# Optimization experiments

Measured on AMD Instinct MI355X. Metric: run time of the kernel, lower is better.

The kernel has to match this reference:

```python
import jax, jax.numpy as jnp
import numpy as np

N = 20000
E = 320000
IN_FEAT = 256
HID = 256
OUT_FEAT = 128


def setup_inputs() -> dict:
    key = jax.random.key(0)
    ks = jax.random.split(key, 10)
    inp = {
        "x": jax.random.normal(ks[0], (N, IN_FEAT), dtype=jnp.float32),
        "edge_src": jax.random.randint(ks[1], (E,), 0, N, dtype=jnp.int32),
        "edge_dst": jax.random.randint(ks[2], (E,), 0, N, dtype=jnp.int32),
        "edge_w": jax.random.uniform(ks[3], (E,), dtype=jnp.float32),
        # params (Linear weights stored as [out, in], torch convention)
        "W_emb": jax.random.normal(ks[4], (HID, IN_FEAT), dtype=jnp.float32) / np.sqrt(IN_FEAT),
        "W_gc1": jax.random.normal(ks[5], (HID, 2 * HID), dtype=jnp.float32) / np.sqrt(2 * HID),
        "b_gc1": jnp.zeros((HID,), dtype=jnp.float32),
        "W_gc2": jax.random.normal(ks[6], (HID, 2 * HID), dtype=jnp.float32) / np.sqrt(2 * HID),
        "b_gc2": jnp.zeros((HID,), dtype=jnp.float32),
        "W_fc": jax.random.normal(ks[7], (OUT_FEAT, HID), dtype=jnp.float32) / np.sqrt(HID),
    }
    return inp


def reference(x, edge_src, edge_dst, edge_w, W_emb, W_gc1, b_gc1, W_gc2, b_gc2, W_fc):
    n = x.shape[0]

    def adj_mul(h):
        msgs = h[edge_src] * edge_w[:, None]           # [E, hid]
        return jax.ops.segment_sum(msgs, edge_dst, num_segments=n)

    def gconv(h, W, b):
        cat = jnp.concatenate([h, adj_mul(h)], axis=1)  # [N, 2*hid]
        return cat @ W.T + b

    h = x @ W_emb.T                                    # embedding (no bias)
    h = h + jax.nn.relu(gconv(h, W_gc1, b_gc1))        # residual (dropout = eval identity)
    h = h + jax.nn.relu(gconv(h, W_gc2, b_gc2))
    out = h @ W_fc.T                                   # fc_last (no bias)
    out = out / jnp.sqrt(jnp.sum(out * out, axis=1, keepdims=True))
    return out
```

## Files before the change

### kernel.cpp

```cpp
#include <hip/hip_runtime.h>
#include <math.h>

#define N_NODES 20000
#define E_EDGES 320000
#define HID 256
#define OUT_FEAT 128
#define MPAD 20224
#define CAP 64

#define BK 64
#define LSTR 72
#define ISTR 80
#define TSTR 264

typedef __attribute__((ext_vector_type(8))) __bf16 bf16x8;
typedef __attribute__((ext_vector_type(4))) float floatx4;
typedef __attribute__((ext_vector_type(4))) int intx4;

__device__ __forceinline__ void write_int8_shadow64(
    const __bf16 (*tile)[TSTR], int row0, int tid,
    unsigned char* __restrict__ h8, float* __restrict__ scl) {
    const int row = tid >> 3;
    const int seg = tid & 7;
    float vals[32];
    float mx = 0.f;
#pragma unroll
    for (int j = 0; j < 32; j++) {
        float v = (float)tile[row][seg * 32 + j];
        vals[j] = v;
        mx = fmaxf(mx, fabsf(v));
    }
#pragma unroll
    for (int m = 1; m <= 4; m <<= 1) mx = fmaxf(mx, __shfl_xor(mx, m));
    const float enc = mx > 0.f ? 127.f / mx : 0.f;
    unsigned int pk[8];
#pragma unroll
    for (int g = 0; g < 8; g++) {
        unsigned int wd = 0;
#pragma unroll
        for (int j = 0; j < 4; j++) {
            int q = (int)rintf(vals[g * 4 + j] * enc);
            q = q > 127 ? 127 : (q < -127 ? -127 : q);
            wd |= ((unsigned int)(q & 0xff)) << (8 * j);
        }
        pk[g] = wd;
    }
    unsigned char* dstp = h8 + (size_t)(row0 + row) * HID + seg * 32;
    *(int4*)dstp        = make_int4(pk[0], pk[1], pk[2], pk[3]);
    *(int4*)(dstp + 16) = make_int4(pk[4], pk[5], pk[6], pk[7]);
    if (seg == 0) scl[row0 + row] = mx * (1.f / 127.f);
}

__device__ __forceinline__ void write_int8_shadow32(
    const __bf16 (*tile)[TSTR], int row0, int tid,
    unsigned char* __restrict__ h8, float* __restrict__ scl) {
    const int row = tid >> 4;
    const int seg = tid & 15;
    float vals[16];
    float mx = 0.f;
#pragma unroll
    for (int j = 0; j < 16; j++) {
        float v = (float)tile[row][seg * 16 + j];
        vals[j] = v;
        mx = fmaxf(mx, fabsf(v));
    }
#pragma unroll
    for (int m = 1; m <= 8; m <<= 1) mx = fmaxf(mx, __shfl_xor(mx, m));
    const float enc = mx > 0.f ? 127.f / mx : 0.f;
    unsigned int pk[4];
#pragma unroll
    for (int g = 0; g < 4; g++) {
        unsigned int wd = 0;
#pragma unroll
        for (int j = 0; j < 4; j++) {
            int q = (int)rintf(vals[g * 4 + j] * enc);
            q = q > 127 ? 127 : (q < -127 ? -127 : q);
            wd |= ((unsigned int)(q & 0xff)) << (8 * j);
        }
        pk[g] = wd;
    }
    unsigned char* dstp = h8 + (size_t)(row0 + row) * HID + seg * 16;
    *(int4*)dstp = make_int4(pk[0], pk[1], pk[2], pk[3]);
    if (seg == 0) scl[row0 + row] = mx * (1.f / 127.f);
}

__device__ __forceinline__ void agg_step16(
    const int2* __restrict__ ep, int cnt, int jb, int lh,
    const unsigned char* __restrict__ h8in, const float* __restrict__ sclin,
    float (&acc)[8]) {
    int4 eh[8];
#pragma unroll
    for (int u = 0; u < 8; u++) eh[u] = *(const int4*)(ep + jb + u * 2);
    int si[16]; float ws[16];
#pragma unroll
    for (int u = 0; u < 8; u++) {
        const bool m0 = (jb + u * 2)     < cnt;
        const bool m1 = (jb + u * 2 + 1) < cnt;
        si[u * 2]     = m0 ? eh[u].x : 0;
        ws[u * 2]     = m0 ? __int_as_float(eh[u].y) : 0.f;
        si[u * 2 + 1] = m1 ? eh[u].z : 0;
        ws[u * 2 + 1] = m1 ? __int_as_float(eh[u].w) : 0.f;
    }
#pragma unroll
    for (int u = 0; u < 16; u++) ws[u] *= sclin[si[u]];
    uint2 hv[16];
#pragma unroll
    for (int u = 0; u < 16; u++)
        hv[u] = *(const uint2*)(h8in + (size_t)si[u] * HID + lh * 8);
#pragma unroll
    for (int u = 0; u < 16; u++) {
        const unsigned int a = hv[u].x, b = hv[u].y;
        const float w = ws[u];
        acc[0] = fmaf(w, (float)(int)(signed char)(a),       acc[0]);
        acc[1] = fmaf(w, (float)(int)(signed char)(a >> 8),  acc[1]);
        acc[2] = fmaf(w, (float)(int)(signed char)(a >> 16), acc[2]);
        acc[3] = fmaf(w, (float)(int)(signed char)(a >> 24), acc[3]);
        acc[4] = fmaf(w, (float)(int)(signed char)(b),       acc[4]);
        acc[5] = fmaf(w, (float)(int)(signed char)(b >> 8),  acc[5]);
        acc[6] = fmaf(w, (float)(int)(signed char)(b >> 16), acc[6]);
        acc[7] = fmaf(w, (float)(int)(signed char)(b >> 24), acc[7]);
    }
}


#define EMB_BLK 316
#define SCAT_BLK 625
#define CONVL_BLK 40
#define CONVR_BLK 64

__global__ __launch_bounds__(512) void front_kernel(
    const float* __restrict__ x, const float* __restrict__ wembf,
    __bf16* __restrict__ hb0, unsigned char* __restrict__ h8, float* __restrict__ scl,
    const int* __restrict__ src, const int* __restrict__ dst,
    const float* __restrict__ w, int* __restrict__ counts, int2* __restrict__ edges,
    const float* __restrict__ w1f, const float* __restrict__ w2f, const float* __restrict__ wfcf,
    __bf16* __restrict__ w1l, __bf16* __restrict__ w2l, __bf16* __restrict__ wfcb,
    unsigned char* __restrict__ w1r8, unsigned char* __restrict__ w2r8,
    float* __restrict__ w1rs, float* __restrict__ w2rs)
{
    __shared__ char smem[64 * 144 + 256 * 144];
    const int bid = blockIdx.x;
    const int tid = threadIdx.x;

    if (bid < EMB_BLK) {
        __bf16* As = (__bf16*)smem;
        __bf16* Bs = (__bf16*)(smem + 64 * 144);
        const int row0 = bid * 64;
        const int wv = tid >> 6, l = tid & 63, lr = l & 15, lq = l >> 4;
        const int wm = wv & 1, wn4 = wv >> 1;

        floatx4 acc[2][4];
#pragma unroll
        for (int i = 0; i < 2; i++)
#pragma unroll
            for (int j = 0; j < 4; j++) acc[i][j] = (floatx4){0.f, 0.f, 0.f, 0.f};

        const int srow = tid >> 3;
        const int skq = (tid & 7) * 8;

        for (int kc = 0; kc < 256; kc += BK) {
            {
                int grow = row0 + srow;
                float4 v0 = make_float4(0.f, 0.f, 0.f, 0.f), v1 = v0;
                if (grow < N_NODES) {
                    const float* xp = x + (size_t)grow * HID + kc + skq;
                    v0 = *(const float4*)xp;
                    v1 = *(const float4*)(xp + 4);
                }
                bf16x8 o;
                o[0] = (__bf16)v0.x; o[1] = (__bf16)v0.y; o[2] = (__bf16)v0.z; o[3] = (__bf16)v0.w;
                o[4] = (__bf16)v1.x; o[5] = (__bf16)v1.y; o[6] = (__bf16)v1.z; o[7] = (__bf16)v1.w;
                *(bf16x8*)&As[srow * LSTR + skq] = o;
            }
#pragma unroll
            for (int r = 0; r < 4; r++) {
                int row = r * 64 + srow;
                const float* wp = wembf + (size_t)row * 256 + kc + skq;
                float4 v0 = *(const float4*)wp;
                float4 v1 = *(const float4*)(wp + 4);
                bf16x8 o;
                o[0] = (__bf16)v0.x; o[1] = (__bf16)v0.y; o[2] = (__bf16)v0.z; o[3] = (__bf16)v0.w;
                o[4] = (__bf16)v1.x; o[5] = (__bf16)v1.y; o[6] = (__bf16)v1.z; o[7] = (__bf16)v1.w;
                *(bf16x8*)&Bs[row * LSTR + skq] = o;
            }
            __syncthreads();
#pragma unroll
            for (int s = 0; s < 2; s++) {
                bf16x8 af[2], bfr[4];
#pragma unroll
                for (int mt = 0; mt < 2; mt++)
                    af[mt] = *(const bf16x8*)&As[(wm * 32 + mt * 16 + lr) * LSTR + s * 32 + lq * 8];
#pragma unroll
                for (int nt = 0; nt < 4; nt++)
                    bfr[nt] = *(const bf16x8*)&Bs[(wn4 * 64 + nt * 16 + lr) * LSTR + s * 32 + lq * 8];
#pragma unroll
                for (int mt = 0; mt < 2; mt++)
#pragma unroll
                    for (int nt = 0; nt < 4; nt++)
                        acc[mt][nt] = __builtin_amdgcn_mfma_f32_16x16x32_bf16(af[mt], bfr[nt], acc[mt][nt], 0, 0, 0);
            }
            __syncthreads();
        }
        __bf16 (*tile)[TSTR] = (__bf16(*)[TSTR])smem;
#pragma unroll
        for (int nt = 0; nt < 4; nt++) {
            const int col = wn4 * 64 + nt * 16 + lr;
#pragma unroll
            for (int mt = 0; mt < 2; mt++) {
                const int lrow = wm * 32 + mt * 16 + lq * 4;
#pragma unroll
                for (int r = 0; r < 4; r++) {
                    float v = acc[mt][nt][r];
                    hb0[(size_t)(row0 + lrow + r) * HID + col] = (__bf16)v;
                    tile[lrow + r][col] = (__bf16)v;
                }
            }
        }
        __syncthreads();
        write_int8_shadow64(tile, row0, tid, h8, scl);
    } else if (bid < EMB_BLK + SCAT_BLK) {
        int e = (bid - EMB_BLK) * 512 + tid;
        int d = dst[e];
        int p = atomicAdd(&counts[d], 1);
        edges[(size_t)d * CAP + p] = make_int2(src[e], __float_as_int(w[e]));
    } else if (bid < EMB_BLK + SCAT_BLK + CONVL_BLK) {
        const size_t gi = ((size_t)(bid - EMB_BLK - SCAT_BLK) * 512 + tid) * 8;
        const float* sp; __bf16* dp;
        if (gi < 65536) {
            size_t row = gi >> 8, k = gi & 255;
            sp = w1f + row * 512 + k; dp = w1l + gi;
        } else if (gi < 131072) {
            size_t off = gi - 65536, row = off >> 8, k = off & 255;
            sp = w2f + row * 512 + k; dp = w2l + off;
        } else {
            size_t off = gi - 131072;
            sp = wfcf + off; dp = wfcb + off;
        }
        float4 v0 = *(const float4*)sp;
        float4 v1 = *(const float4*)(sp + 4);
        bf16x8 o;
        o[0] = (__bf16)v0.x; o[1] = (__bf16)v0.y; o[2] = (__bf16)v0.z; o[3] = (__bf16)v0.w;
        o[4] = (__bf16)v1.x; o[5] = (__bf16)v1.y; o[6] = (__bf16)v1.z; o[7] = (__bf16)v1.w;
        *(bf16x8*)dp = o;
    } else {
        const int gw = (bid - EMB_BLK - SCAT_BLK - CONVL_BLK) * 8 + (tid >> 6);
        const int lane = tid & 63;
        const float* Wsrc = (gw < 256) ? w1f : w2f;
        unsigned char* d8 = (gw < 256) ? w1r8 : w2r8;
        float* ds = (gw < 256) ? w1rs : w2rs;
        const int r = gw & 255;
        float4 v = *(const float4*)(Wsrc + (size_t)r * 512 + 256 + lane * 4);
        float mx = fmaxf(fmaxf(fabsf(v.x), fabsf(v.y)), fmaxf(fabsf(v.z), fabsf(v.w)));
#pragma unroll
        for (int m = 1; m <= 32; m <<= 1) mx = fmaxf(mx, __shfl_xor(mx, m));
        const float enc = mx > 0.f ? 127.f / mx : 0.f;
        unsigned int wd = 0;
        float vv[4] = {v.x, v.y, v.z, v.w};
#pragma unroll
        for (int j = 0; j < 4; j++) {
            int q = (int)rintf(vv[j] * enc);
            q = q > 127 ? 127 : (q < -127 ? -127 : q);
            wd |= ((unsigned int)(q & 0xff)) << (8 * j);
        }
        *(unsigned int*)(d8 + (size_t)r * 256 + lane * 4) = wd;
        if (lane == 0) ds[r] = mx * (1.f / 127.f);
    }
}


#define GBM 32
#define AGG_BYTES (4 * GBM * ISTR)
#define ASCL_OFF  AGG_BYTES
#define GEMM_OFF  (AGG_BYTES + 128)
#define TILE_BYTES (GBM * TSTR * 2)

template <bool LAST>
__global__ __launch_bounds__(512, 4) void gconv_kernel(
    const __bf16* __restrict__ hp,
    const unsigned char* __restrict__ h8in, const float* __restrict__ sclin,
    const int* __restrict__ counts, const int2* __restrict__ edges,
    const __bf16* __restrict__ Wl,
    const unsigned char* __restrict__ Wr8, const float* __restrict__ Wrs,
    const float* __restrict__ bias,
    __bf16* __restrict__ hn, unsigned char* __restrict__ h8out, float* __restrict__ sclout,
    const __bf16* __restrict__ Wfc, float* __restrict__ outp)
{
    __shared__ char smem[GEMM_OFF + TILE_BYTES];
    char* As8 = smem;
    float* asclL = (float*)(smem + ASCL_OFF);
    const int tid = threadIdx.x;
    const int row0 = blockIdx.x * GBM;
    const int wv = tid >> 6, l = tid & 63, lr = l & 15, lq = l >> 4;
    const int wm = wv & 1, wn4 = wv >> 1;

    {
        const int hw = tid >> 5;
        const int lh = tid & 31;
#pragma unroll 1
        for (int rr = 0; rr < 2; ++rr) {
            const int j = hw * 2 + rr;
            const int d = row0 + j;
            const int cnt = counts[d];
            const int2* ep = edges + (size_t)d * CAP;
            const int iters = (cnt + 15) >> 4;
            float acc[8] = {0.f, 0.f, 0.f, 0.f, 0.f, 0.f, 0.f, 0.f};
#pragma unroll 1
            for (int it = 0; it < iters; ++it)
                agg_step16(ep, cnt, it * 16, lh, h8in, sclin, acc);

            float mx = 0.f;
#pragma unroll
            for (int q = 0; q < 8; q++) mx = fmaxf(mx, fabsf(acc[q]));
#pragma unroll
            for (int m = 1; m <= 16; m <<= 1) mx = fmaxf(mx, __shfl_xor(mx, m));
            const float enc = mx > 0.f ? 127.f / mx : 0.f;
            unsigned int w0 = 0, w1v = 0;
#pragma unroll
            for (int jj = 0; jj < 4; jj++) {
                int q0 = (int)rintf(acc[jj] * enc);
                q0 = q0 > 127 ? 127 : (q0 < -127 ? -127 : q0);
                w0 |= ((unsigned int)(q0 & 0xff)) << (8 * jj);
                int q1 = (int)rintf(acc[4 + jj] * enc);
                q1 = q1 > 127 ? 127 : (q1 < -127 ? -127 : q1);
                w1v |= ((unsigned int)(q1 & 0xff)) << (8 * jj);
            }
            *(uint2*)&As8[(((lh >> 3) * GBM) + j) * ISTR + (lh & 7) * 8] = make_uint2(w0, w1v);
            if (lh == 0) asclL[j] = mx * (1.f / 127.f);
        }
    }

    floatx4 acc[4];
    intx4 acc8[4];
#pragma unroll
    for (int j = 0; j < 4; j++) {
        acc[j] = (floatx4){0.f, 0.f, 0.f, 0.f};
        acc8[j] = (intx4){0, 0, 0, 0};
    }

#pragma unroll
    for (int kc = 0; kc < 256; kc += BK) {
#pragma unroll
        for (int s = 0; s < 2; s++) {
            const int k0 = kc + s * 32 + lq * 8;
            bf16x8 af = *(const bf16x8*)(hp + (size_t)(row0 + wm * 16 + lr) * HID + k0);
            bf16x8 bfr[4];
#pragma unroll
            for (int nt = 0; nt < 4; nt++)
                bfr[nt] = *(const bf16x8*)(Wl + (size_t)(wn4 * 64 + nt * 16 + lr) * 256 + k0);
#pragma unroll
            for (int nt = 0; nt < 4; nt++)
                acc[nt] = __builtin_amdgcn_mfma_f32_16x16x32_bf16(af, bfr[nt], acc[nt], 0, 0, 0);
        }
    }

    __syncthreads();

#pragma unroll
    for (int kc = 0; kc < 256; kc += BK) {
        intx4 a8 = *(const intx4*)&As8[(((kc >> 6) * GBM) + wm * 16 + lr) * ISTR + lq * 16];
        intx4 b8[4];
#pragma unroll
        for (int nt = 0; nt < 4; nt++)
            b8[nt] = *(const intx4*)(Wr8 + (size_t)(wn4 * 64 + nt * 16 + lr) * 256 + kc + lq * 16);
#pragma unroll
        for (int nt = 0; nt < 4; nt++)
            acc8[nt] = __builtin_amdgcn_mfma_i32_16x16x64_i8(a8, b8[nt], acc8[nt], 0, 0, 0);
    }

    __bf16 (*tile)[TSTR] = (__bf16(*)[TSTR])(smem + GEMM_OFF);
#pragma unroll
    for (int nt = 0; nt < 4; nt++) {
        const int col = wn4 * 64 + nt * 16 + lr;
        const float b = bias[col];
        const float wrc = Wrs[col];
#pragma unroll
        for (int r = 0; r < 4; r++) {
            const int lrow = wm * 16 + lq * 4 + r;
            const int row = row0 + lrow;
            float gem = acc[nt][r] + (float)acc8[nt][r] * (asclL[lrow] * wrc);
            float res = (float)hp[(size_t)row * HID + col];
            float v = res + fmaxf(gem + b, 0.f);
            if (!LAST) hn[(size_t)row * HID + col] = (__bf16)v;
            tile[lrow][col] = (__bf16)v;
        }
    }
    __syncthreads();

    if (!LAST) {
        write_int8_shadow32(tile, row0, tid, h8out, sclout);
    } else if (wv < 2) {
        floatx4 facc[8];
#pragma unroll
        for (int j = 0; j < 8; j++) facc[j] = (floatx4){0.f, 0.f, 0.f, 0.f};
#pragma unroll
        for (int kt = 0; kt < 256; kt += 32) {
            bf16x8 a = *(const bf16x8*)&tile[wv * 16 + lr][kt + lq * 8];
            bf16x8 bf8[8];
#pragma unroll
            for (int nt = 0; nt < 8; nt++)
                bf8[nt] = *(const bf16x8*)(Wfc + (size_t)(nt * 16 + lr) * 256 + kt + lq * 8);
#pragma unroll
            for (int nt = 0; nt < 8; nt++)
                facc[nt] = __builtin_amdgcn_mfma_f32_16x16x32_bf16(a, bf8[nt], facc[nt], 0, 0, 0);
        }
        float s[4];
#pragma unroll
        for (int r = 0; r < 4; r++) {
            float t = 0.f;
#pragma unroll
            for (int nt = 0; nt < 8; nt++) t = fmaf(facc[nt][r], facc[nt][r], t);
            s[r] = t;
        }
#pragma unroll
        for (int mask = 1; mask <= 8; mask <<= 1) {
#pragma unroll
            for (int r = 0; r < 4; r++) s[r] += __shfl_xor(s[r], mask);
        }
        float inv[4];
#pragma unroll
        for (int r = 0; r < 4; r++) inv[r] = rsqrtf(s[r]);
#pragma unroll
        for (int r = 0; r < 4; r++) {
            int row = row0 + wv * 16 + lq * 4 + r;
            if (row >= N_NODES) continue;
#pragma unroll
            for (int nt = 0; nt < 8; nt++)
                outp[(size_t)row * OUT_FEAT + nt * 16 + lr] = facc[nt][r] * inv[r];
        }
    }
}


extern "C" void kernel_launch(void* const* d_in, const int* in_sizes, int n_in,
                              void* d_out, int out_size, void* d_ws, size_t ws_size,
                              hipStream_t stream) {
    const float* x        = (const float*)d_in[0];
    const int*   edge_src = (const int*)d_in[1];
    const int*   edge_dst = (const int*)d_in[2];
    const float* edge_w   = (const float*)d_in[3];
    const float* W_emb    = (const float*)d_in[4];
    const float* W_gc1    = (const float*)d_in[5];
    const float* b_gc1    = (const float*)d_in[6];
    const float* W_gc2    = (const float*)d_in[7];
    const float* b_gc2    = (const float*)d_in[8];
    const float* W_fc     = (const float*)d_in[9];
    float* out = (float*)d_out;

    char* p = (char*)d_ws;
    const size_t HROW = (size_t)MPAD * HID;
    __bf16* hb0   = (__bf16*)p;             p += HROW * 2;
    __bf16* hb1   = (__bf16*)p;             p += HROW * 2;
    unsigned char* h8a = (unsigned char*)p; p += HROW;
    float*  scla  = (float*)p;              p += (size_t)MPAD * 4;
    unsigned char* h8b = (unsigned char*)p; p += HROW;
    float*  sclb  = (float*)p;              p += (size_t)MPAD * 4;
    __bf16* w1l   = (__bf16*)p;             p += 65536 * 2;
    __bf16* w2l   = (__bf16*)p;             p += 65536 * 2;
    __bf16* wfcb  = (__bf16*)p;             p += 32768 * 2;
    unsigned char* w1r8 = (unsigned char*)p; p += 65536;
    unsigned char* w2r8 = (unsigned char*)p; p += 65536;
    float*  w1rs  = (float*)p;              p += 256 * 4;
    float*  w2rs  = (float*)p;              p += 256 * 4;
    int2*   edges = (int2*)p;               p += (size_t)N_NODES * CAP * 8;
    int*    counts = (int*)p;               p += (size_t)MPAD * 4;

    hipMemsetAsync(counts, 0, (size_t)MPAD * 4, stream);

    front_kernel<<<EMB_BLK + SCAT_BLK + CONVL_BLK + CONVR_BLK, 512, 0, stream>>>(
        x, W_emb, hb0, h8a, scla, edge_src, edge_dst, edge_w, counts, edges,
        W_gc1, W_gc2, W_fc, w1l, w2l, wfcb, w1r8, w2r8, w1rs, w2rs);

    gconv_kernel<false><<<MPAD / GBM, 512, 0, stream>>>(
        hb0, h8a, scla, counts, edges, w1l, w1r8, w1rs, b_gc1,
        hb1, h8b, sclb, nullptr, nullptr);

    gconv_kernel<true><<<MPAD / GBM, 512, 0, stream>>>(
        hb1, h8b, sclb, counts, edges, w2l, w2r8, w2rs, b_gc2,
        nullptr, nullptr, nullptr, wfcb, out);
}
```

Before: 237.3 us.

## Warp-specialize gconv: half the waves aggregate edges while others run the bf16 GEMM

The 512-thread block is split so waves 4-7 do the sparse int8 edge aggregation (four rows each) and stage the residual rows of h into shared memory, while waves 0-3 run the identity-half bf16 GEMM over two M-tiles each. This lets gather latency overlap with MFMA work instead of running the two in sequence. The int8 GEMM and epilogue are then done by waves 0-3 only, reading the residual from shared memory rather than global. The hn output is written with vectorized coalesced stores from the tile. The cost is that each half of the block now carries twice the work per wave, and the GEMM waves hold more accumulator registers.

```diff
diff --git a/kernel.cpp b/kernel.cpp
--- a/kernel.cpp
+++ b/kernel.cpp
@@ -288,105 +288,134 @@
     __shared__ char smem[GEMM_OFF + TILE_BYTES];
     char* As8 = smem;
     float* asclL = (float*)(smem + ASCL_OFF);
+    __bf16 (*tile)[TSTR] = (__bf16(*)[TSTR])(smem + GEMM_OFF);
     const int tid = threadIdx.x;
     const int row0 = blockIdx.x * GBM;
     const int wv = tid >> 6, l = tid & 63, lr = l & 15, lq = l >> 4;
-    const int wm = wv & 1, wn4 = wv >> 1;
-
-    {
-        const int hw = tid >> 5;
+
+    floatx4 acc[2][4];
+    intx4 acc8[2][4];
+#pragma unroll
+    for (int i = 0; i < 2; i++)
+#pragma unroll
+        for (int j = 0; j < 4; j++) {
+            acc[i][j] = (floatx4){0.f, 0.f, 0.f, 0.f};
+            acc8[i][j] = (intx4){0, 0, 0, 0};
+        }
+
+    if (wv >= 4) {
+        const int hw = (tid - 256) >> 5;
         const int lh = tid & 31;
 #pragma unroll 1
-        for (int rr = 0; rr < 2; ++rr) {
-            const int j = hw * 2 + rr;
+        for (int rr = 0; rr < 4; ++rr) {
+            const int j = hw * 4 + rr;
             const int d = row0 + j;
             const int cnt = counts[d];
             const int2* ep = edges + (size_t)d * CAP;
             const int iters = (cnt + 15) >> 4;
-            float acc[8] = {0.f, 0.f, 0.f, 0.f, 0.f, 0.f, 0.f, 0.f};
+            float acca[8] = {0.f, 0.f, 0.f, 0.f, 0.f, 0.f, 0.f, 0.f};
 #pragma unroll 1
             for (int it = 0; it < iters; ++it)
-                agg_step16(ep, cnt, it * 16, lh, h8in, sclin, acc);
+                agg_step16(ep, cnt, it * 16, lh, h8in, sclin, acca);
 
             float mx = 0.f;
 #pragma unroll
-            for (int q = 0; q < 8; q++) mx = fmaxf(mx, fabsf(acc[q]));
+            for (int q = 0; q < 8; q++) mx = fmaxf(mx, fabsf(acca[q]));
 #pragma unroll
             for (int m = 1; m <= 16; m <<= 1) mx = fmaxf(mx, __shfl_xor(mx, m));
             const float enc = mx > 0.f ? 127.f / mx : 0.f;
             unsigned int w0 = 0, w1v = 0;
 #pragma unroll
             for (int jj = 0; jj < 4; jj++) {
-                int q0 = (int)rintf(acc[jj] * enc);
+                int q0 = (int)rintf(acca[jj] * enc);
                 q0 = q0 > 127 ? 127 : (q0 < -127 ? -127 : q0);
                 w0 |= ((unsigned int)(q0 & 0xff)) << (8 * jj);
-                int q1 = (int)rintf(acc[4 + jj] * enc);
+                int q1 = (int)rintf(acca[4 + jj] * enc);
                 q1 = q1 > 127 ? 127 : (q1 < -127 ? -127 : q1);
                 w1v |= ((unsigned int)(q1 & 0xff)) << (8 * jj);
             }
             *(uint2*)&As8[(((lh >> 3) * GBM) + j) * ISTR + (lh & 7) * 8] = make_uint2(w0, w1v);
             if (lh == 0) asclL[j] = mx * (1.f / 127.f);
         }
-    }
-
-    floatx4 acc[4];
-    intx4 acc8[4];
-#pragma unroll
-    for (int j = 0; j < 4; j++) {
-        acc[j] = (floatx4){0.f, 0.f, 0.f, 0.f};
-        acc8[j] = (intx4){0, 0, 0, 0};
-    }
-
-#pragma unroll
-    for (int kc = 0; kc < 256; kc += BK) {
-#pragma unroll
-        for (int s = 0; s < 2; s++) {
-            const int k0 = kc + s * 32 + lq * 8;
-            bf16x8 af = *(const bf16x8*)(hp + (size_t)(row0 + wm * 16 + lr) * HID + k0);
-            bf16x8 bfr[4];
+        {
+            const int t = tid - 256;
+            const int row = t >> 3;
+            const int sg = (t & 7) * 32;
+            const __bf16* rp = hp + (size_t)(row0 + row) * HID + sg;
+#pragma unroll
+            for (int g = 0; g < 4; g++)
+                *(bf16x8*)&tile[row][sg + g * 8] = *(const bf16x8*)(rp + g * 8);
+        }
+    } else {
+#pragma unroll
+        for (int kc = 0; kc < 256; kc += BK) {
+#pragma unroll
+            for (int s = 0; s < 2; s++) {
+                const int k0 = kc + s * 32 + lq * 8;
+                bf16x8 af[2], bfr[4];
+#pragma unroll
+                for (int mt = 0; mt < 2; mt++)
+                    af[mt] = *(const bf16x8*)(hp + (size_t)(row0 + mt * 16 + lr) * HID + k0);
+#pragma unroll
+                for (int nt = 0; nt < 4; nt++)
+                    bfr[nt] = *(const bf16x8*)(Wl + (size_t)(wv * 64 + nt * 16 + lr) * 256 + k0);
+#pragma unroll
+                for (int mt = 0; mt < 2; mt++)
+#pragma unroll
+                    for (int nt = 0; nt < 4; nt++)
+                        acc[mt][nt] = __builtin_amdgcn_mfma_f32_16x16x32_bf16(af[mt], bfr[nt], acc[mt][nt], 0, 0, 0);
+            }
+        }
+    }
+
+    __syncthreads();
+
+    if (wv < 4) {
+#pragma unroll
+        for (int kc = 0; kc < 256; kc += BK) {
+            intx4 a8[2], b8[4];
+#pragma unroll
+            for (int mt = 0; mt < 2; mt++)
+                a8[mt] = *(const intx4*)&As8[(((kc >> 6) * GBM) + mt * 16 + lr) * ISTR + lq * 16];
 #pragma unroll
             for (int nt = 0; nt < 4; nt++)
-                bfr[nt] = *(const bf16x8*)(Wl + (size_t)(wn4 * 64 + nt * 16 + lr) * 256 + k0);
-#pragma unroll
-            for (int nt = 0; nt < 4; nt++)
-                acc[nt] = __builtin_amdgcn_mfma_f32_16x16x32_bf16(af, bfr[nt], acc[nt], 0, 0, 0);
+                b8[nt] = *(const intx4*)(Wr8 + (size_t)(wv * 64 + nt * 16 + lr) * 256 + kc + lq * 16);
+#pragma unroll
+            for (int mt = 0; mt < 2; mt++)
+#pragma unroll
+                for (int nt = 0; nt < 4; nt++)
+                    acc8[mt][nt] = __builtin_amdgcn_mfma_i32_16x16x64_i8(a8[mt], b8[nt], acc8[mt][nt], 0, 0, 0);
+        }
+
+#pragma unroll
+        for (int nt = 0; nt < 4; nt++) {
+            const int col = wv * 64 + nt * 16 + lr;
+            const float b = bias[col];
+            const float wrc = Wrs[col];
+#pragma unroll
+            for (int mt = 0; mt < 2; mt++) {
+                const int lrow = mt * 16 + lq * 4;
+#pragma unroll
+                for (int r = 0; r < 4; r++) {
+                    float gem = acc[mt][nt][r] + (float)acc8[mt][nt][r] * (asclL[lrow + r] * wrc);
+                    float res = (float)tile[lrow + r][col];
+                    float v = res + fmaxf(gem + b, 0.f);
+                    tile[lrow + r][col] = (__bf16)v;
+                }
+            }
         }
     }
 
     __syncthreads();
 
-#pragma unroll
-    for (int kc = 0; kc < 256; kc += BK) {
-        intx4 a8 = *(const intx4*)&As8[(((kc >> 6) * GBM) + wm * 16 + lr) * ISTR + lq * 16];
-        intx4 b8[4];
-#pragma unroll
-        for (int nt = 0; nt < 4; nt++)
-            b8[nt] = *(const intx4*)(Wr8 + (size_t)(wn4 * 64 + nt * 16 + lr) * 256 + kc + lq * 16);
-#pragma unroll
-        for (int nt = 0; nt < 4; nt++)
-            acc8[nt] = __builtin_amdgcn_mfma_i32_16x16x64_i8(a8, b8[nt], acc8[nt], 0, 0, 0);
-    }
-
-    __bf16 (*tile)[TSTR] = (__bf16(*)[TSTR])(smem + GEMM_OFF);
-#pragma unroll
-    for (int nt = 0; nt < 4; nt++) {
-        const int col = wn4 * 64 + nt * 16 + lr;
-        const float b = bias[col];
-        const float wrc = Wrs[col];
-#pragma unroll
-        for (int r = 0; r < 4; r++) {
-            const int lrow = wm * 16 + lq * 4 + r;
-            const int row = row0 + lrow;
-            float gem = acc[nt][r] + (float)acc8[nt][r] * (asclL[lrow] * wrc);
-            float res = (float)hp[(size_t)row * HID + col];
-            float v = res + fmaxf(gem + b, 0.f);
-            if (!LAST) hn[(size_t)row * HID + col] = (__bf16)v;
-            tile[lrow][col] = (__bf16)v;
-        }
-    }
-    __syncthreads();
-
     if (!LAST) {
+        {
+            const int row = tid >> 4;
+            const int col = (tid & 15) * 16;
+            __bf16* dp = hn + (size_t)(row0 + row) * HID + col;
+            *(bf16x8*)dp       = *(const bf16x8*)&tile[row][col];
+            *(bf16x8*)(dp + 8) = *(const bf16x8*)&tile[row][col + 8];
+        }
         write_int8_shadow32(tile, row0, tid, h8out, sclout);
     } else if (wv < 2) {
         floatx4 facc[8];
```

Result: faster. 220.9 us (-6.9%).
